# Kernel tuning notes

Measured on AMD Instinct MI355X. Metric: run time of the kernel, lower is better.

Reference implementation:

```python
import jax, jax.numpy as jnp
import numpy as np

N = 32000      # total nodes (16 graphs x 2000 nodes)
B = 16         # batch of graphs
NPG = N // B   # nodes per graph
K = 1600       # assign_dim (total clusters)
KPG = K // B   # clusters per graph
D = 128        # input_dim == output_feat_dim
E = 512000     # edges (avg degree 16), block-diagonal across graphs


def setup_inputs() -> dict:
    key = jax.random.key(0)
    ks = jax.random.split(key, 12)
    # block-structured edge list: each edge stays within its graph
    epg = E // B
    gid = jnp.repeat(jnp.arange(B, dtype=jnp.int32), epg) * NPG
    src = gid + jax.random.randint(ks[0], (E,), 0, NPG, dtype=jnp.int32)
    dst = gid + jax.random.randint(ks[1], (E,), 0, NPG, dtype=jnp.int32)
    h = jax.random.normal(ks[2], (N, D), dtype=jnp.float32)
    s = 0.05
    return {
        'h': h, 'src': src, 'dst': dst,
        'W1f': jax.random.normal(ks[3], (D, D), jnp.float32) * s,
        'b1f': jnp.zeros((D,), jnp.float32),
        'W2f': jax.random.normal(ks[4], (D, D), jnp.float32) * s,
        'b2f': jnp.zeros((D,), jnp.float32),
        'W1p': jax.random.normal(ks[5], (D, K), jnp.float32) * s,
        'b1p': jnp.zeros((K,), jnp.float32),
        'W2p': jax.random.normal(ks[6], (K, K), jnp.float32) * s,
        'b2p': jnp.zeros((K,), jnp.float32),
    }


def _gin(h, src, dst, W1, b1, W2, b2):
    # mean-aggregate neighbor features, then 2-layer MLP (histocartography GINLayer)
    deg = jax.ops.segment_sum(jnp.ones((src.shape[0],), h.dtype), dst, num_segments=N)
    agg = jax.ops.segment_sum(h[src], dst, num_segments=N)
    agg = agg / jnp.maximum(deg, 1.0)[:, None]
    x = h + agg
    x = jax.nn.relu(x @ W1 + b1)
    x = jax.nn.relu(x @ W2 + b2)
    return x


def _forward(h, src, dst, W1f, b1f, W2f, b2f, W1p, b1p, W2p, b2p):
    feat = _gin(h, src, dst, W1f, b1f, W2f, b2f)            # [N, D]
    assign = _gin(h, src, dst, W1p, b1p, W2p, b2p)          # [N, K]
    # block-diagonal mask: node of graph b can only assign to clusters of graph b
    node_gid = jnp.arange(N, dtype=jnp.int32) // NPG
    col_gid = jnp.arange(K, dtype=jnp.int32) // KPG
    mask = (node_gid[:, None] == col_gid[None, :]).astype(assign.dtype)  # [N, K]
    # masked_softmax(memory_efficient=False): softmax(x*mask)*mask, renormalized
    p = jax.nn.softmax(assign * mask, axis=-1) * mask
    assign = p / (jnp.sum(p, axis=-1, keepdims=True) + 1e-13)
    h_pool = assign.T @ feat                                # [K, D]
    # adj @ assign where adj[dst, src] = 1 (sparse-dense mm via scatter)
    tmp = jax.ops.segment_sum(assign[src], dst, num_segments=N)  # [N, K]
    adj_new = assign.T @ tmp                                # [K, K]
    return adj_new, h_pool


def reference(h, src, dst, W1f, b1f, W2f, b2f, W1p, b1p, W2p, b2p):
    return _forward(h, src, dst, W1f, b1f, W2f, b2f, W1p, b1p, W2p, b2p)
```

## Files before the change

kernel.cpp:

```cpp
#include <hip/hip_runtime.h>

#define N_NODES 32000
#define NPG     2000
#define NGRAPH  16
#define K_ASSIGN 1600
#define KPG     100
#define D_FEAT  128
#define N_EDGES 512000

typedef float f32x4 __attribute__((ext_vector_type(4)));
typedef __bf16 bf16x8 __attribute__((ext_vector_type(8)));

union FragU { unsigned u[4]; bf16x8 v; };

__device__ __forceinline__ float frelu(float v) { return fmaxf(v, 0.0f); }

__device__ __forceinline__ unsigned short f2bf(float f) {
  unsigned u = __float_as_uint(f);
  u += 0x7FFFu + ((u >> 16) & 1u);
  return (unsigned short)(u >> 16);
}
__device__ __forceinline__ float bfLO(unsigned v) { return __uint_as_float(v << 16); }
__device__ __forceinline__ float bfHI(unsigned v) { return __uint_as_float(v & 0xFFFF0000u); }

__global__ __launch_bounds__(256) void prep_all(
    const float* __restrict__ W1f, const float* __restrict__ W2f,
    const float* __restrict__ W1p, const float* __restrict__ W2p,
    unsigned short* __restrict__ o1, unsigned short* __restrict__ o2,
    unsigned short* __restrict__ o3, unsigned short* __restrict__ o4,
    const float* __restrict__ h, unsigned short* __restrict__ h_bf,
    const int* __restrict__ dst, int* __restrict__ cnt) {
  __shared__ float tile[32][33];
  int b = blockIdx.x;
  int t = threadIdx.x;
  if (b >= 6732) {
    int e = (b - 6732) * 256 + t;
    if (e < N_EDGES) atomicAdd(&cnt[dst[e]], 1);
    return;
  }
  if (b >= 2732) {
    int i = (b - 2732) * 256 + t;
    float4 v = ((const float4*)h)[i];
    ushort4 o;
    o.x = f2bf(v.x); o.y = f2bf(v.y); o.z = f2bf(v.z); o.w = f2bf(v.w);
    ((ushort4*)h_bf)[i] = o;
    return;
  }
  const float* in;
  unsigned short* out;
  int R, C, rb;
  if (b < 16)       { in = W1f; out = o1; R = 128;  C = 128;  rb = b; }
  else if (b < 32)  { in = W2f; out = o2; R = 128;  C = 128;  rb = b - 16; }
  else if (b < 232) { in = W1p; out = o3; R = 128;  C = 1600; rb = b - 32; }
  else              { in = W2p; out = o4; R = 1600; C = 1600; rb = b - 232; }
  int ct = C >> 5;
  int bc = rb % ct, br = rb / ct;
  int r0 = br * 32, c0 = bc * 32;
#pragma unroll
  for (int i = 0; i < 4; i++) {
    int r = (t >> 5) + i * 8, c = t & 31;
    tile[r][c] = in[(size_t)(r0 + r) * C + c0 + c];
  }
  __syncthreads();
#pragma unroll
  for (int i = 0; i < 4; i++) {
    int c = (t >> 5) + i * 8, r = t & 31;
    out[(size_t)(c0 + c) * R + r0 + r] = f2bf(tile[r][c]);
  }
}

__global__ __launch_bounds__(1024) void scan_counts(
    const int* __restrict__ cnt, int* __restrict__ rowstart) {
  __shared__ int sums[1024];
  int t = threadIdx.x;
  int base = t * 32;
  int s = 0;
  if (t < 1000)
    for (int i = 0; i < 32; i++) s += cnt[base + i];
  sums[t] = s;
  __syncthreads();
  for (int off = 1; off < 1024; off <<= 1) {
    int v = (t >= off) ? sums[t - off] : 0;
    __syncthreads();
    sums[t] += v;
    __syncthreads();
  }
  if (t < 1000) {
    int run = (t == 0) ? 0 : sums[t - 1];
    for (int i = 0; i < 32; i++) {
      rowstart[base + i] = run;
      run += cnt[base + i];
    }
  }
  if (t == 999) rowstart[32000] = sums[999];
}

__global__ __launch_bounds__(256) void edge_fill(
    const int* __restrict__ src, const int* __restrict__ dst,
    const int* __restrict__ rowstart, int* __restrict__ cursor,
    int* __restrict__ bucket) {
  int e = blockIdx.x * 256 + threadIdx.x;
  if (e < N_EDGES) {
    int d = dst[e];
    int pos = atomicAdd(&cursor[d], 1);
    bucket[rowstart[d] + pos] = src[e];
  }
}

__global__ __launch_bounds__(256) void gin_gather(
    const int* __restrict__ rowstart, const int* __restrict__ bucket,
    const unsigned short* __restrict__ h_bf, unsigned short* __restrict__ x_bf) {
  int bid = (int)(blockIdx.x & 7) * 1000 + (int)(blockIdx.x >> 3);
  int n = bid * 4 + (threadIdx.x >> 6);
  int lane = threadIdx.x & 63;
  int rs = rowstart[n], re = rowstart[n + 1];
  int deg = re - rs;
  const unsigned* hb = (const unsigned*)h_bf;
  unsigned hv = hb[(size_t)n * 64 + lane];
  float ax = 0.f, ay = 0.f;
  for (int base = 0; base < deg; base += 64) {
    int cnt = deg - base;
    if (cnt > 64) cnt = 64;
    int myidx = (lane < cnt) ? bucket[rs + base + lane] : 0;
    int j = 0;
    for (; j + 8 <= cnt; j += 8) {
      int s0 = __shfl(myidx, j + 0), s1 = __shfl(myidx, j + 1);
      int s2 = __shfl(myidx, j + 2), s3 = __shfl(myidx, j + 3);
      int s4 = __shfl(myidx, j + 4), s5 = __shfl(myidx, j + 5);
      int s6 = __shfl(myidx, j + 6), s7 = __shfl(myidx, j + 7);
      unsigned v0 = hb[(size_t)s0 * 64 + lane];
      unsigned v1 = hb[(size_t)s1 * 64 + lane];
      unsigned v2 = hb[(size_t)s2 * 64 + lane];
      unsigned v3 = hb[(size_t)s3 * 64 + lane];
      unsigned v4 = hb[(size_t)s4 * 64 + lane];
      unsigned v5 = hb[(size_t)s5 * 64 + lane];
      unsigned v6 = hb[(size_t)s6 * 64 + lane];
      unsigned v7 = hb[(size_t)s7 * 64 + lane];
      ax += ((bfLO(v0) + bfLO(v1)) + (bfLO(v2) + bfLO(v3))) +
            ((bfLO(v4) + bfLO(v5)) + (bfLO(v6) + bfLO(v7)));
      ay += ((bfHI(v0) + bfHI(v1)) + (bfHI(v2) + bfHI(v3))) +
            ((bfHI(v4) + bfHI(v5)) + (bfHI(v6) + bfHI(v7)));
    }
    for (; j < cnt; j++) {
      int s0 = __shfl(myidx, j);
      unsigned v = hb[(size_t)s0 * 64 + lane];
      ax += bfLO(v);
      ay += bfHI(v);
    }
  }
  float invd = 1.0f / fmaxf((float)deg, 1.0f);
  unsigned o = ((unsigned)f2bf(bfHI(hv) + ay * invd) << 16) |
               f2bf(bfLO(hv) + ax * invd);
  ((unsigned*)x_bf)[(size_t)n * 64 + lane] = o;
}

#define FF_STR 136
#define FA_WS 136
#define FA_PS 72
#define FA_W1OFF 17408
#define FA_W2BASE 34816
#define FA_W2OFF 16128
__global__ __launch_bounds__(512) void feat_assign(
    const unsigned short* __restrict__ x_bf,
    const unsigned short* __restrict__ w1ft, const float* __restrict__ b1f,
    const unsigned short* __restrict__ w2ft, const float* __restrict__ b2f,
    unsigned short* __restrict__ feat_bf,
    const unsigned short* __restrict__ w1t, const float* __restrict__ b1p,
    const unsigned short* __restrict__ w2t, const float* __restrict__ b2p,
    unsigned short* __restrict__ assign_bf) {
  __shared__ __align__(16) unsigned char smem[69632];
  int t = threadIdx.x;
  int w = t >> 6, l = t & 63, lr = l & 15, lg = l >> 4;

  if (blockIdx.x >= 256) {
    unsigned short* xa = (unsigned short*)smem;
    unsigned short* ws = (unsigned short*)(smem + 34816);
    size_t base = (size_t)(blockIdx.x - 256) * 128;

#pragma unroll
    for (int i = 0; i < 4; i++) {
      int fi = t + 512 * i;
      int r = fi >> 4, u8 = (fi & 15) * 8;
      *(uint4*)&xa[r * FF_STR + u8] = *(const uint4*)(x_bf + (base + r) * 128 + u8);
      *(uint4*)&ws[r * FF_STR + u8] = *(const uint4*)(w1ft + (size_t)r * 128 + u8);
    }
    __syncthreads();

    int myrow = 16 * w + lr;
    bf16x8 af[4];
#pragma unroll
    for (int kc = 0; kc < 4; kc++)
      af[kc] = *(bf16x8*)&xa[myrow * FF_STR + 32 * kc + 8 * lg];

    f32x4 p[8];
#pragma unroll
    for (int ntk = 0; ntk < 8; ntk++) {
      p[ntk] = (f32x4){0.f, 0.f, 0.f, 0.f};
      int c = 16 * ntk + lr;
#pragma unroll
      for (int kc = 0; kc < 4; kc++) {
        bf16x8 wf = *(bf16x8*)&ws[c * FF_STR + 32 * kc + 8 * lg];
        p[ntk] = __builtin_amdgcn_mfma_f32_16x16x32_bf16(wf, af[kc], p[ntk], 0, 0, 0);
      }
    }
    __syncthreads();

#pragma unroll
    for (int ntk = 0; ntk < 8; ntk++) {
      int kk0 = 16 * ntk + 4 * lg;
      float4 b1 = *(const float4*)(b1f + kk0);
      ushort4 pk;
      pk.x = f2bf(frelu(p[ntk][0] + b1.x));
      pk.y = f2bf(frelu(p[ntk][1] + b1.y));
      pk.z = f2bf(frelu(p[ntk][2] + b1.z));
      pk.w = f2bf(frelu(p[ntk][3] + b1.w));
      *(ushort4*)&xa[myrow * FF_STR + kk0] = pk;
    }
#pragma unroll
    for (int i = 0; i < 4; i++) {
      int fi = t + 512 * i;
      int r = fi >> 4, u8 = (fi & 15) * 8;
      *(uint4*)&ws[r * FF_STR + u8] = *(const uint4*)(w2ft + (size_t)r * 128 + u8);
    }
    __syncthreads();

    bf16x8 a2[4];
#pragma unroll
    for (int kc = 0; kc < 4; kc++)
      a2[kc] = *(bf16x8*)&xa[myrow * FF_STR + 32 * kc + 8 * lg];
#pragma unroll
    for (int nt = 0; nt < 8; nt++) {
      f32x4 q = (f32x4){0.f, 0.f, 0.f, 0.f};
      int c = 16 * nt + lr;
#pragma unroll
      for (int kc = 0; kc < 4; kc++) {
        bf16x8 wf = *(bf16x8*)&ws[c * FF_STR + 32 * kc + 8 * lg];
        q = __builtin_amdgcn_mfma_f32_16x16x32_bf16(wf, a2[kc], q, 0, 0, 0);
      }
      int c0 = 16 * nt + 4 * lg;
      float4 b2 = *(const float4*)(b2f + c0);
      ushort4 pk;
      pk.x = f2bf(frelu(q[0] + b2.x));
      pk.y = f2bf(frelu(q[1] + b2.y));
      pk.z = f2bf(frelu(q[2] + b2.z));
      pk.w = f2bf(frelu(q[3] + b2.w));
      *(ushort4*)&feat_bf[(base + myrow) * 128 + c0] = pk;
    }
    return;
  }

  unsigned short* xt = (unsigned short*)smem;
  int g = blockIdx.x >> 4;
  int row0 = (blockIdx.x & 15) << 7;
  int n0 = g * NPG + row0;

#pragma unroll
  for (int i = 0; i < 4; i++) {
    int fi = t + 512 * i;
    int r = fi >> 4, u8 = (fi & 15) * 8;
    uint4 v = make_uint4(0, 0, 0, 0);
    if (row0 + r < NPG) v = *(const uint4*)(x_bf + (size_t)(n0 + r) * 128 + u8);
    *(uint4*)&xt[r * FA_WS + u8] = v;
  }
  __syncthreads();

  int rh = w >> 1, h = w & 1;

  bf16x8 af[2][4];
#pragma unroll
  for (int ct = 0; ct < 2; ct++)
#pragma unroll
    for (int kc = 0; kc < 4; kc++)
      af[ct][kc] =
          *(bf16x8*)&xt[(32 * rh + 16 * ct + lr) * FA_WS + 32 * kc + 8 * lg];
  __syncthreads();

  {
    unsigned short* w1s = (unsigned short*)smem;
    unsigned short* w2s = (unsigned short*)(smem + FA_W2BASE);
#pragma unroll
    for (int i = 0; i < 2; i++) {
      int fi = t + 512 * i;
      int c = fi >> 4, u8 = (fi & 15) * 8;
      *(uint4*)&w1s[c * FA_WS + u8] = *(const uint4*)(w1t + (size_t)c * 128 + u8);
    }
#pragma unroll
    for (int i = 0; i < 2; i++) {
      int fi = t + 512 * i;
      if (fi < 896) {
        int c = fi >> 3, u8 = (fi & 7) * 8;
        uint4 v = make_uint4(0, 0, 0, 0);
        if (c < KPG)
          v = *(const uint4*)(w2t + (size_t)(g * KPG + c) * K_ASSIGN + u8);
        *(uint4*)&w2s[c * FA_PS + u8] = v;
      }
    }
  }
  __syncthreads();

  f32x4 acc[7][2];
#pragma unroll
  for (int i = 0; i < 7; i++) {
    acc[i][0] = (f32x4){0.f, 0.f, 0.f, 0.f};
    acc[i][1] = (f32x4){0.f, 0.f, 0.f, 0.f};
  }

  for (int cch = 0; cch < 25; cch++) {
    int cur = cch & 1;
    int k0 = cch * 64;
    const unsigned short* w1c = (const unsigned short*)(smem + cur * FA_W1OFF);
    const unsigned short* w2c =
        (const unsigned short*)(smem + FA_W2BASE + cur * FA_W2OFF);
    bool pf = (cch < 24);
    uint4 rA[2], rB[2];
    if (pf) {
      int k1 = k0 + 64;
#pragma unroll
      for (int i = 0; i < 2; i++) {
        int fi = t + 512 * i;
        int c = fi >> 4, u8 = (fi & 15) * 8;
        rA[i] = *(const uint4*)(w1t + (size_t)(k1 + c) * 128 + u8);
      }
#pragma unroll
      for (int i = 0; i < 2; i++) {
        int fi = t + 512 * i;
        rB[i] = make_uint4(0, 0, 0, 0);
        if (fi < 896) {
          int c = fi >> 3, u8 = (fi & 7) * 8;
          if (c < KPG)
            rB[i] = *(const uint4*)(w2t + (size_t)(g * KPG + c) * K_ASSIGN +
                                    k1 + u8);
        }
      }
    }

    f32x4 p[2][2];
    __builtin_amdgcn_s_setprio(1);
#pragma unroll
    for (int nt2 = 0; nt2 < 2; nt2++) {
      p[nt2][0] = (f32x4){0.f, 0.f, 0.f, 0.f};
      p[nt2][1] = (f32x4){0.f, 0.f, 0.f, 0.f};
      int nt = 2 * h + nt2;
#pragma unroll
      for (int kc = 0; kc < 4; kc++) {
        bf16x8 wf = *(bf16x8*)&w1c[(16 * nt + lr) * FA_WS + 32 * kc + 8 * lg];
        p[nt2][0] = __builtin_amdgcn_mfma_f32_16x16x32_bf16(wf, af[0][kc],
                                                            p[nt2][0], 0, 0, 0);
        p[nt2][1] = __builtin_amdgcn_mfma_f32_16x16x32_bf16(wf, af[1][kc],
                                                            p[nt2][1], 0, 0, 0);
      }
    }
    __builtin_amdgcn_s_setprio(0);
    unsigned q[2][2][2];
#pragma unroll
    for (int nt2 = 0; nt2 < 2; nt2++) {
      int kkb = k0 + 16 * (2 * h + nt2) + 4 * lg;
      float4 b1 = *(const float4*)(b1p + kkb);
#pragma unroll
      for (int ct = 0; ct < 2; ct++) {
        float r0 = frelu(p[nt2][ct][0] + b1.x);
        float r1 = frelu(p[nt2][ct][1] + b1.y);
        float r2 = frelu(p[nt2][ct][2] + b1.z);
        float r3 = frelu(p[nt2][ct][3] + b1.w);
        q[nt2][ct][0] = ((unsigned)f2bf(r1) << 16) | f2bf(r0);
        q[nt2][ct][1] = ((unsigned)f2bf(r3) << 16) | f2bf(r2);
      }
    }
    int sA = lr + 32 * (lg & 1);
    int sB = sA + 16;
    bool hi = (lg >= 2);
    FragU pa[2];
#pragma unroll
    for (int ct = 0; ct < 2; ct++) {
      unsigned a0 = (unsigned)__shfl((int)q[0][ct][0], sA, 64);
      unsigned b0 = (unsigned)__shfl((int)q[1][ct][0], sA, 64);
      unsigned a1 = (unsigned)__shfl((int)q[0][ct][1], sA, 64);
      unsigned b1u = (unsigned)__shfl((int)q[1][ct][1], sA, 64);
      unsigned a2 = (unsigned)__shfl((int)q[0][ct][0], sB, 64);
      unsigned b2u = (unsigned)__shfl((int)q[1][ct][0], sB, 64);
      unsigned a3 = (unsigned)__shfl((int)q[0][ct][1], sB, 64);
      unsigned b3u = (unsigned)__shfl((int)q[1][ct][1], sB, 64);
      pa[ct].u[0] = hi ? b0 : a0;
      pa[ct].u[1] = hi ? b1u : a1;
      pa[ct].u[2] = hi ? b2u : a2;
      pa[ct].u[3] = hi ? b3u : a3;
    }
    if (pf) {
      unsigned short* w1n = (unsigned short*)(smem + (cur ^ 1) * FA_W1OFF);
      unsigned short* w2n =
          (unsigned short*)(smem + FA_W2BASE + (cur ^ 1) * FA_W2OFF);
#pragma unroll
      for (int i = 0; i < 2; i++) {
        int fi = t + 512 * i;
        int c = fi >> 4, u8 = (fi & 15) * 8;
        *(uint4*)&w1n[c * FA_WS + u8] = rA[i];
      }
#pragma unroll
      for (int i = 0; i < 2; i++) {
        int fi = t + 512 * i;
        if (fi < 896) {
          int c = fi >> 3, u8 = (fi & 7) * 8;
          *(uint4*)&w2n[c * FA_PS + u8] = rB[i];
        }
      }
    }
    __builtin_amdgcn_s_setprio(1);
#pragma unroll
    for (int ct2 = 0; ct2 < 7; ct2++) {
      bf16x8 wv = *(bf16x8*)&w2c[(16 * ct2 + lr) * FA_PS + 32 * h + 8 * lg];
      acc[ct2][0] = __builtin_amdgcn_mfma_f32_16x16x32_bf16(wv, pa[0].v,
                                                            acc[ct2][0], 0, 0, 0);
      acc[ct2][1] = __builtin_amdgcn_mfma_f32_16x16x32_bf16(wv, pa[1].v,
                                                            acc[ct2][1], 0, 0, 0);
    }
    __builtin_amdgcn_s_setprio(0);
    __syncthreads();
  }

  float* red = (float*)smem;
  if (h == 1) {
#pragma unroll
    for (int ct2 = 0; ct2 < 7; ct2++)
#pragma unroll
      for (int ct = 0; ct < 2; ct++)
        *(f32x4*)&red[((rh * 14 + ct2 * 2 + ct) * 64 + l) * 4] = acc[ct2][ct];
  }
  __syncthreads();
  if (h == 0) {
#pragma unroll
    for (int ct2 = 0; ct2 < 7; ct2++)
#pragma unroll
      for (int ct = 0; ct < 2; ct++)
        acc[ct2][ct] += *(f32x4*)&red[((rh * 14 + ct2 * 2 + ct) * 64 + l) * 4];

#pragma unroll
    for (int ct = 0; ct < 2; ct++) {
      int xrow = row0 + 32 * rh + 16 * ct + lr;
      float v[7][4];
      float m = 0.0f;
#pragma unroll
      for (int ct2 = 0; ct2 < 7; ct2++) {
        int col0 = 16 * ct2 + 4 * lg;
        if (col0 < KPG) {
          float4 b2 = *(const float4*)(b2p + g * KPG + col0);
          v[ct2][0] = frelu(acc[ct2][ct][0] + b2.x);
          v[ct2][1] = frelu(acc[ct2][ct][1] + b2.y);
          v[ct2][2] = frelu(acc[ct2][ct][2] + b2.z);
          v[ct2][3] = frelu(acc[ct2][ct][3] + b2.w);
          m = fmaxf(m, fmaxf(fmaxf(v[ct2][0], v[ct2][1]),
                             fmaxf(v[ct2][2], v[ct2][3])));
        }
      }
      m = fmaxf(m, __shfl_xor(m, 16, 64));
      m = fmaxf(m, __shfl_xor(m, 32, 64));
      float s = 0.0f;
#pragma unroll
      for (int ct2 = 0; ct2 < 7; ct2++) {
        int col0 = 16 * ct2 + 4 * lg;
        if (col0 < KPG) {
          v[ct2][0] = expf(v[ct2][0] - m);
          v[ct2][1] = expf(v[ct2][1] - m);
          v[ct2][2] = expf(v[ct2][2] - m);
          v[ct2][3] = expf(v[ct2][3] - m);
          s += (v[ct2][0] + v[ct2][1]) + (v[ct2][2] + v[ct2][3]);
        }
      }
      s += __shfl_xor(s, 16, 64);
      s += __shfl_xor(s, 32, 64);
      float denom = s + (float)(K_ASSIGN - KPG) * expf(-m);
      float scale = 1.0f / (s + 1e-13f * denom);
      if (xrow < NPG) {
#pragma unroll
        for (int ct2 = 0; ct2 < 7; ct2++) {
          int col0 = 16 * ct2 + 4 * lg;
          if (col0 < KPG) {
            ushort4 pk;
            pk.x = f2bf(v[ct2][0] * scale);
            pk.y = f2bf(v[ct2][1] * scale);
            pk.z = f2bf(v[ct2][2] * scale);
            pk.w = f2bf(v[ct2][3] * scale);
            *(ushort4*)(assign_bf + ((size_t)g * NPG + xrow) * KPG + col0) = pk;
          }
        }
      }
    }
  }
}

__global__ __launch_bounds__(256) void tmp_gather(
    const int* __restrict__ rowstart, const int* __restrict__ bucket,
    const unsigned short* __restrict__ assign_bf, unsigned short* __restrict__ tmp_bf) {
  int bid = (int)(blockIdx.x & 7) * 1000 + (int)(blockIdx.x >> 3);
  int n = bid * 4 + (threadIdx.x >> 6);
  int lane = threadIdx.x & 63;
  int rs = rowstart[n], re = rowstart[n + 1];
  int deg = re - rs;
  int lc = (lane < 50) ? lane : 0;
  const unsigned* ab = (const unsigned*)assign_bf;
  float ax = 0.f, ay = 0.f;
  for (int base = 0; base < deg; base += 64) {
    int cnt = deg - base;
    if (cnt > 64) cnt = 64;
    int myidx = (lane < cnt) ? bucket[rs + base + lane] : 0;
    int j = 0;
    for (; j + 8 <= cnt; j += 8) {
      int s0 = __shfl(myidx, j + 0), s1 = __shfl(myidx, j + 1);
      int s2 = __shfl(myidx, j + 2), s3 = __shfl(myidx, j + 3);
      int s4 = __shfl(myidx, j + 4), s5 = __shfl(myidx, j + 5);
      int s6 = __shfl(myidx, j + 6), s7 = __shfl(myidx, j + 7);
      unsigned v0 = ab[(size_t)s0 * 50 + lc];
      unsigned v1 = ab[(size_t)s1 * 50 + lc];
      unsigned v2 = ab[(size_t)s2 * 50 + lc];
      unsigned v3 = ab[(size_t)s3 * 50 + lc];
      unsigned v4 = ab[(size_t)s4 * 50 + lc];
      unsigned v5 = ab[(size_t)s5 * 50 + lc];
      unsigned v6 = ab[(size_t)s6 * 50 + lc];
      unsigned v7 = ab[(size_t)s7 * 50 + lc];
      ax += ((bfLO(v0) + bfLO(v1)) + (bfLO(v2) + bfLO(v3))) +
            ((bfLO(v4) + bfLO(v5)) + (bfLO(v6) + bfLO(v7)));
      ay += ((bfHI(v0) + bfHI(v1)) + (bfHI(v2) + bfHI(v3))) +
            ((bfHI(v4) + bfHI(v5)) + (bfHI(v6) + bfHI(v7)));
    }
    for (; j < cnt; j++) {
      int s0 = __shfl(myidx, j);
      unsigned v = ab[(size_t)s0 * 50 + lc];
      ax += bfLO(v);
      ay += bfHI(v);
    }
  }
  if (lane < 50) {
    unsigned o = ((unsigned)f2bf(ay) << 16) | f2bf(ax);
    ((unsigned*)tmp_bf)[(size_t)n * 50 + lane] = o;
  }
}

#define PA_STR 72
#define PA_CHN 128
__global__ __launch_bounds__(256) void pool_adj_mfma(
    const unsigned short* __restrict__ assign_bf,
    const unsigned short* __restrict__ feat_bf,
    const unsigned short* __restrict__ tmp_bf,
    float* __restrict__ out_adj, float* __restrict__ out_hpool) {
  __shared__ __align__(16) unsigned short as[112 * PA_STR];
  __shared__ __align__(16) unsigned short bs[128 * PA_STR];
  bool is_pool = blockIdx.x < 256;
  int bb = is_pool ? blockIdx.x : blockIdx.x - 256;
  int g = bb >> 4, ch = bb & 15;
  int nbase = ch * PA_CHN;
  int lim = NPG - nbase;
  if (lim > PA_CHN) lim = PA_CHN;
  int t = threadIdx.x;
  int w = t >> 6, l = t & 63, lr = l & 15, lg = l >> 4;
  const unsigned* au = (const unsigned*)assign_bf;
  const unsigned* fu = (const unsigned*)feat_bf;
  const unsigned* tu = (const unsigned*)tmp_bf;

  for (int i = t; i < 12 * PA_STR; i += 256) as[100 * PA_STR + i] = 0;
  for (int i = t; i < 28 * PA_STR; i += 256) bs[100 * PA_STR + i] = 0;

  f32x4 acc[7][2];
#pragma unroll
  for (int i = 0; i < 7; i++) {
    acc[i][0] = (f32x4){0.f, 0.f, 0.f, 0.f};
    acc[i][1] = (f32x4){0.f, 0.f, 0.f, 0.f};
  }

  for (int kt = 0; kt < 2; kt++) {
    int nt0 = kt * 64;
    __syncthreads();
#pragma unroll
    for (int i = 0; i < 13; i++) {
      int idx = t + 256 * i;
      if (idx < 3200) {
        int r = idx / 50, cu = idx % 50;
        int nl = nt0 + r;
        unsigned v = 0;
        if (nl < lim) v = au[(size_t)(g * NPG + nbase + nl) * 50 + cu];
        as[(2 * cu) * PA_STR + r] = (unsigned short)(v & 0xFFFFu);
        as[(2 * cu + 1) * PA_STR + r] = (unsigned short)(v >> 16);
      }
    }
    if (is_pool) {
#pragma unroll
      for (int i = 0; i < 16; i++) {
        int idx = t + 256 * i;
        int r = idx >> 6, cu = idx & 63;
        int nl = nt0 + r;
        unsigned v = 0;
        if (nl < lim) v = fu[(size_t)(g * NPG + nbase + nl) * 64 + cu];
        bs[(2 * cu) * PA_STR + r] = (unsigned short)(v & 0xFFFFu);
        bs[(2 * cu + 1) * PA_STR + r] = (unsigned short)(v >> 16);
      }
    } else {
#pragma unroll
      for (int i = 0; i < 13; i++) {
        int idx = t + 256 * i;
        if (idx < 3200) {
          int r = idx / 50, cu = idx % 50;
          int nl = nt0 + r;
          unsigned v = 0;
          if (nl < lim) v = tu[(size_t)(g * NPG + nbase + nl) * 50 + cu];
          bs[(2 * cu) * PA_STR + r] = (unsigned short)(v & 0xFFFFu);
          bs[(2 * cu + 1) * PA_STR + r] = (unsigned short)(v >> 16);
        }
      }
    }
    __syncthreads();
#pragma unroll
    for (int kc = 0; kc < 2; kc++) {
      bf16x8 afr[7];
#pragma unroll
      for (int mt = 0; mt < 7; mt++)
        afr[mt] = *(bf16x8*)&as[(16 * mt + lr) * PA_STR + 32 * kc + 8 * lg];
#pragma unroll
      for (int nt2 = 0; nt2 < 2; nt2++) {
        int nt = 2 * w + nt2;
        bf16x8 bfr = *(bf16x8*)&bs[(16 * nt + lr) * PA_STR + 32 * kc + 8 * lg];
#pragma unroll
        for (int mt = 0; mt < 7; mt++)
          acc[mt][nt2] =
              __builtin_amdgcn_mfma_f32_16x16x32_bf16(afr[mt], bfr, acc[mt][nt2], 0, 0, 0);
      }
    }
  }

  if (is_pool) {
#pragma unroll
    for (int mt = 0; mt < 7; mt++)
#pragma unroll
      for (int nt2 = 0; nt2 < 2; nt2++) {
        int nt = 2 * w + nt2;
#pragma unroll
        for (int r = 0; r < 4; r++) {
          int m = 16 * mt + 4 * lg + r;
          if (m < KPG)
            atomicAdd(out_hpool + ((size_t)g * KPG + m) * 128 + 16 * nt + lr,
                      acc[mt][nt2][r]);
        }
      }
  } else {
#pragma unroll
    for (int mt = 0; mt < 7; mt++)
#pragma unroll
      for (int nt2 = 0; nt2 < 2; nt2++) {
        int nt = 2 * w + nt2;
        if (nt < 7) {
          int k2 = 16 * nt + lr;
          if (k2 < KPG) {
#pragma unroll
            for (int r = 0; r < 4; r++) {
              int m = 16 * mt + 4 * lg + r;
              if (m < KPG)
                atomicAdd(out_adj + ((size_t)g * KPG + m) * K_ASSIGN + g * KPG + k2,
                          acc[mt][nt2][r]);
            }
          }
        }
      }
  }
}

extern "C" void kernel_launch(void* const* d_in, const int* in_sizes, int n_in,
                              void* d_out, int out_size, void* d_ws,
                              size_t ws_size, hipStream_t stream) {
  (void)in_sizes; (void)n_in; (void)ws_size;
  const float* h   = (const float*)d_in[0];
  const int*   src = (const int*)d_in[1];
  const int*   dst = (const int*)d_in[2];
  const float* W1f = (const float*)d_in[3];
  const float* b1f = (const float*)d_in[4];
  const float* W2f = (const float*)d_in[5];
  const float* b2f = (const float*)d_in[6];
  const float* W1p = (const float*)d_in[7];
  const float* b1p = (const float*)d_in[8];
  const float* W2p = (const float*)d_in[9];
  const float* b2p = (const float*)d_in[10];

  float* out_adj   = (float*)d_out;
  float* out_hpool = out_adj + (size_t)K_ASSIGN * K_ASSIGN;

  char* ws = (char*)d_ws;
  int* deg_cnt  = (int*)(ws + 0);
  int* rowstart = (int*)(ws + 128000);
  int* cursor   = (int*)(ws + 256032);
  int* bucket   = (int*)(ws + 384032);
  unsigned short* h_bf      = (unsigned short*)(ws + 2432032);
  unsigned short* x_bf      = (unsigned short*)(ws + 10624032);
  unsigned short* feat_bf   = (unsigned short*)(ws + 18816032);
  unsigned short* assign_bf = (unsigned short*)(ws + 27008032);
  unsigned short* tmp_bf    = (unsigned short*)(ws + 33408032);
  unsigned short* w1f_t     = (unsigned short*)(ws + 39808032);
  unsigned short* w2f_t     = (unsigned short*)(ws + 39840800);
  unsigned short* w1p_t     = (unsigned short*)(ws + 39873568);
  unsigned short* w2p_t     = (unsigned short*)(ws + 40283168);

  hipMemsetAsync(deg_cnt, 0, 128000, stream);
  hipMemsetAsync(cursor, 0, 128000, stream);
  hipMemsetAsync(d_out, 0, (size_t)out_size * sizeof(float), stream);

  prep_all<<<8732, 256, 0, stream>>>(W1f, W2f, W1p, W2p, w1f_t, w2f_t, w1p_t,
                                     w2p_t, h, h_bf, dst, deg_cnt);

  scan_counts<<<1, 1024, 0, stream>>>(deg_cnt, rowstart);
  edge_fill<<<N_EDGES / 256, 256, 0, stream>>>(src, dst, rowstart, cursor, bucket);

  gin_gather<<<N_NODES / 4, 256, 0, stream>>>(rowstart, bucket, h_bf, x_bf);

  feat_assign<<<256 + N_NODES / 128, 512, 0, stream>>>(
      x_bf, w1f_t, b1f, w2f_t, b2f, feat_bf,
      w1p_t, b1p, w2p_t, b2p, assign_bf);

  tmp_gather<<<N_NODES / 4, 256, 0, stream>>>(rowstart, bucket, assign_bf, tmp_bf);

  pool_adj_mfma<<<512, 256, 0, stream>>>(assign_bf, feat_bf, tmp_bf,
                                         out_adj, out_hpool);
}
```

Baseline: 216.5 us.

## Fuse neighbor-mean gather into feat_assign, dropping the separate x_bf pass

Removes the standalone gin_gather kernel and its x_bf buffer. Each feat_assign block now computes its own rows of x (h plus the mean of its neighbors) directly into shared memory before the MLP matmuls, with each wave gathering 16 rows. This saves one kernel launch and a global write and re-read of x. In exchange the feat and assign blocks each redo the same gather (256 + 250 blocks over the same nodes), and the gather now runs inside a kernel that has 512 threads per block and a large shared-memory footprint, which may reduce latency hiding.

```diff
diff --git a/kernel.cpp b/kernel.cpp
--- a/kernel.cpp
+++ b/kernel.cpp
@@ -23,99 +23,11 @@
 __device__ __forceinline__ float bfLO(unsigned v) { return __uint_as_float(v << 16); }
 __device__ __forceinline__ float bfHI(unsigned v) { return __uint_as_float(v & 0xFFFF0000u); }
 
-__global__ __launch_bounds__(256) void prep_all(
-    const float* __restrict__ W1f, const float* __restrict__ W2f,
-    const float* __restrict__ W1p, const float* __restrict__ W2p,
-    unsigned short* __restrict__ o1, unsigned short* __restrict__ o2,
-    unsigned short* __restrict__ o3, unsigned short* __restrict__ o4,
-    const float* __restrict__ h, unsigned short* __restrict__ h_bf,
-    const int* __restrict__ dst, int* __restrict__ cnt) {
-  __shared__ float tile[32][33];
-  int b = blockIdx.x;
-  int t = threadIdx.x;
-  if (b >= 6732) {
-    int e = (b - 6732) * 256 + t;
-    if (e < N_EDGES) atomicAdd(&cnt[dst[e]], 1);
-    return;
-  }
-  if (b >= 2732) {
-    int i = (b - 2732) * 256 + t;
-    float4 v = ((const float4*)h)[i];
-    ushort4 o;
-    o.x = f2bf(v.x); o.y = f2bf(v.y); o.z = f2bf(v.z); o.w = f2bf(v.w);
-    ((ushort4*)h_bf)[i] = o;
-    return;
-  }
-  const float* in;
-  unsigned short* out;
-  int R, C, rb;
-  if (b < 16)       { in = W1f; out = o1; R = 128;  C = 128;  rb = b; }
-  else if (b < 32)  { in = W2f; out = o2; R = 128;  C = 128;  rb = b - 16; }
-  else if (b < 232) { in = W1p; out = o3; R = 128;  C = 1600; rb = b - 32; }
-  else              { in = W2p; out = o4; R = 1600; C = 1600; rb = b - 232; }
-  int ct = C >> 5;
-  int bc = rb % ct, br = rb / ct;
-  int r0 = br * 32, c0 = bc * 32;
-#pragma unroll
-  for (int i = 0; i < 4; i++) {
-    int r = (t >> 5) + i * 8, c = t & 31;
-    tile[r][c] = in[(size_t)(r0 + r) * C + c0 + c];
-  }
-  __syncthreads();
-#pragma unroll
-  for (int i = 0; i < 4; i++) {
-    int c = (t >> 5) + i * 8, r = t & 31;
-    out[(size_t)(c0 + c) * R + r0 + r] = f2bf(tile[r][c]);
-  }
-}
-
-__global__ __launch_bounds__(1024) void scan_counts(
-    const int* __restrict__ cnt, int* __restrict__ rowstart) {
-  __shared__ int sums[1024];
-  int t = threadIdx.x;
-  int base = t * 32;
-  int s = 0;
-  if (t < 1000)
-    for (int i = 0; i < 32; i++) s += cnt[base + i];
-  sums[t] = s;
-  __syncthreads();
-  for (int off = 1; off < 1024; off <<= 1) {
-    int v = (t >= off) ? sums[t - off] : 0;
-    __syncthreads();
-    sums[t] += v;
-    __syncthreads();
-  }
-  if (t < 1000) {
-    int run = (t == 0) ? 0 : sums[t - 1];
-    for (int i = 0; i < 32; i++) {
-      rowstart[base + i] = run;
-      run += cnt[base + i];
-    }
-  }
-  if (t == 999) rowstart[32000] = sums[999];
-}
-
-__global__ __launch_bounds__(256) void edge_fill(
-    const int* __restrict__ src, const int* __restrict__ dst,
-    const int* __restrict__ rowstart, int* __restrict__ cursor,
-    int* __restrict__ bucket) {
-  int e = blockIdx.x * 256 + threadIdx.x;
-  if (e < N_EDGES) {
-    int d = dst[e];
-    int pos = atomicAdd(&cursor[d], 1);
-    bucket[rowstart[d] + pos] = src[e];
-  }
-}
-
-__global__ __launch_bounds__(256) void gin_gather(
-    const int* __restrict__ rowstart, const int* __restrict__ bucket,
-    const unsigned short* __restrict__ h_bf, unsigned short* __restrict__ x_bf) {
-  int bid = (int)(blockIdx.x & 7) * 1000 + (int)(blockIdx.x >> 3);
-  int n = bid * 4 + (threadIdx.x >> 6);
-  int lane = threadIdx.x & 63;
+__device__ __forceinline__ unsigned gather_x_u32(
+    int n, int lane, const int* __restrict__ rowstart,
+    const int* __restrict__ bucket, const unsigned* __restrict__ hb) {
   int rs = rowstart[n], re = rowstart[n + 1];
   int deg = re - rs;
-  const unsigned* hb = (const unsigned*)h_bf;
   unsigned hv = hb[(size_t)n * 64 + lane];
   float ax = 0.f, ay = 0.f;
   for (int base = 0; base < deg; base += 64) {
@@ -149,9 +61,92 @@
     }
   }
   float invd = 1.0f / fmaxf((float)deg, 1.0f);
-  unsigned o = ((unsigned)f2bf(bfHI(hv) + ay * invd) << 16) |
-               f2bf(bfLO(hv) + ax * invd);
-  ((unsigned*)x_bf)[(size_t)n * 64 + lane] = o;
+  return ((unsigned)f2bf(bfHI(hv) + ay * invd) << 16) |
+         f2bf(bfLO(hv) + ax * invd);
+}
+
+__global__ __launch_bounds__(256) void prep_all(
+    const float* __restrict__ W1f, const float* __restrict__ W2f,
+    const float* __restrict__ W1p, const float* __restrict__ W2p,
+    unsigned short* __restrict__ o1, unsigned short* __restrict__ o2,
+    unsigned short* __restrict__ o3, unsigned short* __restrict__ o4,
+    const float* __restrict__ h, unsigned short* __restrict__ h_bf,
+    const int* __restrict__ dst, int* __restrict__ cnt) {
+  __shared__ float tile[32][33];
+  int b = blockIdx.x;
+  int t = threadIdx.x;
+  if (b >= 6732) {
+    int e = (b - 6732) * 256 + t;
+    if (e < N_EDGES) atomicAdd(&cnt[dst[e]], 1);
+    return;
+  }
+  if (b >= 2732) {
+    int i = (b - 2732) * 256 + t;
+    float4 v = ((const float4*)h)[i];
+    ushort4 o;
+    o.x = f2bf(v.x); o.y = f2bf(v.y); o.z = f2bf(v.z); o.w = f2bf(v.w);
+    ((ushort4*)h_bf)[i] = o;
+    return;
+  }
+  const float* in;
+  unsigned short* out;
+  int R, C, rb;
+  if (b < 16)       { in = W1f; out = o1; R = 128;  C = 128;  rb = b; }
+  else if (b < 32)  { in = W2f; out = o2; R = 128;  C = 128;  rb = b - 16; }
+  else if (b < 232) { in = W1p; out = o3; R = 128;  C = 1600; rb = b - 32; }
+  else              { in = W2p; out = o4; R = 1600; C = 1600; rb = b - 232; }
+  int ct = C >> 5;
+  int bc = rb % ct, br = rb / ct;
+  int r0 = br * 32, c0 = bc * 32;
+#pragma unroll
+  for (int i = 0; i < 4; i++) {
+    int r = (t >> 5) + i * 8, c = t & 31;
+    tile[r][c] = in[(size_t)(r0 + r) * C + c0 + c];
+  }
+  __syncthreads();
+#pragma unroll
+  for (int i = 0; i < 4; i++) {
+    int c = (t >> 5) + i * 8, r = t & 31;
+    out[(size_t)(c0 + c) * R + r0 + r] = f2bf(tile[r][c]);
+  }
+}
+
+__global__ __launch_bounds__(1024) void scan_counts(
+    const int* __restrict__ cnt, int* __restrict__ rowstart) {
+  __shared__ int sums[1024];
+  int t = threadIdx.x;
+  int base = t * 32;
+  int s = 0;
+  if (t < 1000)
+    for (int i = 0; i < 32; i++) s += cnt[base + i];
+  sums[t] = s;
+  __syncthreads();
+  for (int off = 1; off < 1024; off <<= 1) {
+    int v = (t >= off) ? sums[t - off] : 0;
+    __syncthreads();
+    sums[t] += v;
+    __syncthreads();
+  }
+  if (t < 1000) {
+    int run = (t == 0) ? 0 : sums[t - 1];
+    for (int i = 0; i < 32; i++) {
+      rowstart[base + i] = run;
+      run += cnt[base + i];
+    }
+  }
+  if (t == 999) rowstart[32000] = sums[999];
+}
+
+__global__ __launch_bounds__(256) void edge_fill(
+    const int* __restrict__ src, const int* __restrict__ dst,
+    const int* __restrict__ rowstart, int* __restrict__ cursor,
+    int* __restrict__ bucket) {
+  int e = blockIdx.x * 256 + threadIdx.x;
+  if (e < N_EDGES) {
+    int d = dst[e];
+    int pos = atomicAdd(&cursor[d], 1);
+    bucket[rowstart[d] + pos] = src[e];
+  }
 }
 
 #define FF_STR 136
@@ -161,7 +156,8 @@
 #define FA_W2BASE 34816
 #define FA_W2OFF 16128
 __global__ __launch_bounds__(512) void feat_assign(
-    const unsigned short* __restrict__ x_bf,
+    const int* __restrict__ rowstart, const int* __restrict__ bucket,
+    const unsigned short* __restrict__ h_bf,
     const unsigned short* __restrict__ w1ft, const float* __restrict__ b1f,
     const unsigned short* __restrict__ w2ft, const float* __restrict__ b2f,
     unsigned short* __restrict__ feat_bf,
@@ -171,6 +167,7 @@
   __shared__ __align__(16) unsigned char smem[69632];
   int t = threadIdx.x;
   int w = t >> 6, l = t & 63, lr = l & 15, lg = l >> 4;
+  const unsigned* hb = (const unsigned*)h_bf;
 
   if (blockIdx.x >= 256) {
     unsigned short* xa = (unsigned short*)smem;
@@ -181,8 +178,12 @@
     for (int i = 0; i < 4; i++) {
       int fi = t + 512 * i;
       int r = fi >> 4, u8 = (fi & 15) * 8;
-      *(uint4*)&xa[r * FF_STR + u8] = *(const uint4*)(x_bf + (base + r) * 128 + u8);
       *(uint4*)&ws[r * FF_STR + u8] = *(const uint4*)(w1ft + (size_t)r * 128 + u8);
+    }
+    for (int j = 0; j < 16; j++) {
+      int r = 16 * w + j;
+      unsigned o = gather_x_u32((int)base + r, l, rowstart, bucket, hb);
+      *(unsigned*)&xa[r * FF_STR + l * 2] = o;
     }
     __syncthreads();
 
@@ -254,13 +255,11 @@
   int row0 = (blockIdx.x & 15) << 7;
   int n0 = g * NPG + row0;
 
-#pragma unroll
-  for (int i = 0; i < 4; i++) {
-    int fi = t + 512 * i;
-    int r = fi >> 4, u8 = (fi & 15) * 8;
-    uint4 v = make_uint4(0, 0, 0, 0);
-    if (row0 + r < NPG) v = *(const uint4*)(x_bf + (size_t)(n0 + r) * 128 + u8);
-    *(uint4*)&xt[r * FA_WS + u8] = v;
+  for (int j = 0; j < 16; j++) {
+    int r = 16 * w + j;
+    unsigned o = 0;
+    if (row0 + r < NPG) o = gather_x_u32(n0 + r, l, rowstart, bucket, hb);
+    *(unsigned*)&xt[r * FA_WS + l * 2] = o;
   }
   __syncthreads();
 
@@ -685,14 +684,13 @@
   int* cursor   = (int*)(ws + 256032);
   int* bucket   = (int*)(ws + 384032);
   unsigned short* h_bf      = (unsigned short*)(ws + 2432032);
-  unsigned short* x_bf      = (unsigned short*)(ws + 10624032);
-  unsigned short* feat_bf   = (unsigned short*)(ws + 18816032);
-  unsigned short* assign_bf = (unsigned short*)(ws + 27008032);
-  unsigned short* tmp_bf    = (unsigned short*)(ws + 33408032);
-  unsigned short* w1f_t     = (unsigned short*)(ws + 39808032);
-  unsigned short* w2f_t     = (unsigned short*)(ws + 39840800);
-  unsigned short* w1p_t     = (unsigned short*)(ws + 39873568);
-  unsigned short* w2p_t     = (unsigned short*)(ws + 40283168);
+  unsigned short* feat_bf   = (unsigned short*)(ws + 10624032);
+  unsigned short* assign_bf = (unsigned short*)(ws + 18816032);
+  unsigned short* tmp_bf    = (unsigned short*)(ws + 25216032);
+  unsigned short* w1f_t     = (unsigned short*)(ws + 31616032);
+  unsigned short* w2f_t     = (unsigned short*)(ws + 31648800);
+  unsigned short* w1p_t     = (unsigned short*)(ws + 31681568);
+  unsigned short* w2p_t     = (unsigned short*)(ws + 32091168);
 
   hipMemsetAsync(deg_cnt, 0, 128000, stream);
   hipMemsetAsync(cursor, 0, 128000, stream);
@@ -704,10 +702,9 @@
   scan_counts<<<1, 1024, 0, stream>>>(deg_cnt, rowstart);
   edge_fill<<<N_EDGES / 256, 256, 0, stream>>>(src, dst, rowstart, cursor, bucket);
 
-  gin_gather<<<N_NODES / 4, 256, 0, stream>>>(rowstart, bucket, h_bf, x_bf);
-
   feat_assign<<<256 + N_NODES / 128, 512, 0, stream>>>(
-      x_bf, w1f_t, b1f, w2f_t, b2f, feat_bf,
+      rowstart, bucket, h_bf,
+      w1f_t, b1f, w2f_t, b2f, feat_bf,
       w1p_t, b1p, w2p_t, b2p, assign_bf);
 
   tmp_gather<<<N_NODES / 4, 256, 0, stream>>>(rowstart, bucket, assign_bf, tmp_bf);
```

Measured after the change: 286.2 us. +32.2%, slower.

## Load GIN weight fragments directly from global memory instead of LDS staging

Applied to the files above, without the earlier changes.

Removes LDS staging and double buffering of the W1/W2 weights in both the feature and assignment MLP paths. Each wave now loads its MFMA weight fragments straight from global memory, relying on L2/cache reuse. This drops most per-chunk __syncthreads and halves shared memory use, which may raise occupancy. The trade-off is redundant global loads per wave and no explicit prefetch, and the reduction is split into two smaller passes.

```diff
diff --git a/kernel.cpp b/kernel.cpp
--- a/kernel.cpp
+++ b/kernel.cpp
@@ -156,10 +156,6 @@
 
 #define FF_STR 136
 #define FA_WS 136
-#define FA_PS 72
-#define FA_W1OFF 17408
-#define FA_W2BASE 34816
-#define FA_W2OFF 16128
 __global__ __launch_bounds__(512) void feat_assign(
     const unsigned short* __restrict__ x_bf,
     const unsigned short* __restrict__ w1ft, const float* __restrict__ b1f,
@@ -168,24 +164,19 @@
     const unsigned short* __restrict__ w1t, const float* __restrict__ b1p,
     const unsigned short* __restrict__ w2t, const float* __restrict__ b2p,
     unsigned short* __restrict__ assign_bf) {
-  __shared__ __align__(16) unsigned char smem[69632];
+  __shared__ __align__(16) unsigned char smem[34816];
   int t = threadIdx.x;
   int w = t >> 6, l = t & 63, lr = l & 15, lg = l >> 4;
 
   if (blockIdx.x >= 256) {
     unsigned short* xa = (unsigned short*)smem;
-    unsigned short* ws = (unsigned short*)(smem + 34816);
     size_t base = (size_t)(blockIdx.x - 256) * 128;
-
-#pragma unroll
-    for (int i = 0; i < 4; i++) {
-      int fi = t + 512 * i;
-      int r = fi >> 4, u8 = (fi & 15) * 8;
+#pragma unroll
+    for (int j = 0; j < 4; j++) {
+      int idx = l + 64 * j;
+      int r = 16 * w + (idx >> 4), u8 = (idx & 15) * 8;
       *(uint4*)&xa[r * FF_STR + u8] = *(const uint4*)(x_bf + (base + r) * 128 + u8);
-      *(uint4*)&ws[r * FF_STR + u8] = *(const uint4*)(w1ft + (size_t)r * 128 + u8);
-    }
-    __syncthreads();
-
+    }
     int myrow = 16 * w + lr;
     bf16x8 af[4];
 #pragma unroll
@@ -195,16 +186,16 @@
     f32x4 p[8];
 #pragma unroll
     for (int ntk = 0; ntk < 8; ntk++) {
+      int c = 16 * ntk + lr;
+      bf16x8 wfr[4];
+#pragma unroll
+      for (int kc = 0; kc < 4; kc++)
+        wfr[kc] = *(const bf16x8*)(w1ft + (size_t)c * 128 + 32 * kc + 8 * lg);
       p[ntk] = (f32x4){0.f, 0.f, 0.f, 0.f};
-      int c = 16 * ntk + lr;
-#pragma unroll
-      for (int kc = 0; kc < 4; kc++) {
-        bf16x8 wf = *(bf16x8*)&ws[c * FF_STR + 32 * kc + 8 * lg];
-        p[ntk] = __builtin_amdgcn_mfma_f32_16x16x32_bf16(wf, af[kc], p[ntk], 0, 0, 0);
-      }
-    }
-    __syncthreads();
-
+#pragma unroll
+      for (int kc = 0; kc < 4; kc++)
+        p[ntk] = __builtin_amdgcn_mfma_f32_16x16x32_bf16(wfr[kc], af[kc], p[ntk], 0, 0, 0);
+    }
 #pragma unroll
     for (int ntk = 0; ntk < 8; ntk++) {
       int kk0 = 16 * ntk + 4 * lg;
@@ -216,27 +207,21 @@
       pk.w = f2bf(frelu(p[ntk][3] + b1.w));
       *(ushort4*)&xa[myrow * FF_STR + kk0] = pk;
     }
-#pragma unroll
-    for (int i = 0; i < 4; i++) {
-      int fi = t + 512 * i;
-      int r = fi >> 4, u8 = (fi & 15) * 8;
-      *(uint4*)&ws[r * FF_STR + u8] = *(const uint4*)(w2ft + (size_t)r * 128 + u8);
-    }
-    __syncthreads();
-
     bf16x8 a2[4];
 #pragma unroll
     for (int kc = 0; kc < 4; kc++)
       a2[kc] = *(bf16x8*)&xa[myrow * FF_STR + 32 * kc + 8 * lg];
 #pragma unroll
     for (int nt = 0; nt < 8; nt++) {
+      int c = 16 * nt + lr;
+      bf16x8 wfr[4];
+#pragma unroll
+      for (int kc = 0; kc < 4; kc++)
+        wfr[kc] = *(const bf16x8*)(w2ft + (size_t)c * 128 + 32 * kc + 8 * lg);
       f32x4 q = (f32x4){0.f, 0.f, 0.f, 0.f};
-      int c = 16 * nt + lr;
-#pragma unroll
-      for (int kc = 0; kc < 4; kc++) {
-        bf16x8 wf = *(bf16x8*)&ws[c * FF_STR + 32 * kc + 8 * lg];
-        q = __builtin_amdgcn_mfma_f32_16x16x32_bf16(wf, a2[kc], q, 0, 0, 0);
-      }
+#pragma unroll
+      for (int kc = 0; kc < 4; kc++)
+        q = __builtin_amdgcn_mfma_f32_16x16x32_bf16(wfr[kc], a2[kc], q, 0, 0, 0);
       int c0 = 16 * nt + 4 * lg;
       float4 b2 = *(const float4*)(b2f + c0);
       ushort4 pk;
@@ -264,7 +249,7 @@
   }
   __syncthreads();
 
-  int rh = w >> 1, h = w & 1;
+  int rh = w >> 1, hh = w & 1;
 
   bf16x8 af[2][4];
 #pragma unroll
@@ -273,30 +258,6 @@
     for (int kc = 0; kc < 4; kc++)
       af[ct][kc] =
           *(bf16x8*)&xt[(32 * rh + 16 * ct + lr) * FA_WS + 32 * kc + 8 * lg];
-  __syncthreads();
-
-  {
-    unsigned short* w1s = (unsigned short*)smem;
-    unsigned short* w2s = (unsigned short*)(smem + FA_W2BASE);
-#pragma unroll
-    for (int i = 0; i < 2; i++) {
-      int fi = t + 512 * i;
-      int c = fi >> 4, u8 = (fi & 15) * 8;
-      *(uint4*)&w1s[c * FA_WS + u8] = *(const uint4*)(w1t + (size_t)c * 128 + u8);
-    }
-#pragma unroll
-    for (int i = 0; i < 2; i++) {
-      int fi = t + 512 * i;
-      if (fi < 896) {
-        int c = fi >> 3, u8 = (fi & 7) * 8;
-        uint4 v = make_uint4(0, 0, 0, 0);
-        if (c < KPG)
-          v = *(const uint4*)(w2t + (size_t)(g * KPG + c) * K_ASSIGN + u8);
-        *(uint4*)&w2s[c * FA_PS + u8] = v;
-      }
-    }
-  }
-  __syncthreads();
 
   f32x4 acc[7][2];
 #pragma unroll
@@ -306,47 +267,23 @@
   }
 
   for (int cch = 0; cch < 25; cch++) {
-    int cur = cch & 1;
     int k0 = cch * 64;
-    const unsigned short* w1c = (const unsigned short*)(smem + cur * FA_W1OFF);
-    const unsigned short* w2c =
-        (const unsigned short*)(smem + FA_W2BASE + cur * FA_W2OFF);
-    bool pf = (cch < 24);
-    uint4 rA[2], rB[2];
-    if (pf) {
-      int k1 = k0 + 64;
-#pragma unroll
-      for (int i = 0; i < 2; i++) {
-        int fi = t + 512 * i;
-        int c = fi >> 4, u8 = (fi & 15) * 8;
-        rA[i] = *(const uint4*)(w1t + (size_t)(k1 + c) * 128 + u8);
-      }
-#pragma unroll
-      for (int i = 0; i < 2; i++) {
-        int fi = t + 512 * i;
-        rB[i] = make_uint4(0, 0, 0, 0);
-        if (fi < 896) {
-          int c = fi >> 3, u8 = (fi & 7) * 8;
-          if (c < KPG)
-            rB[i] = *(const uint4*)(w2t + (size_t)(g * KPG + c) * K_ASSIGN +
-                                    k1 + u8);
-        }
-      }
-    }
-
     f32x4 p[2][2];
     __builtin_amdgcn_s_setprio(1);
 #pragma unroll
     for (int nt2 = 0; nt2 < 2; nt2++) {
+      bf16x8 wfr[4];
+#pragma unroll
+      for (int kc = 0; kc < 4; kc++)
+        wfr[kc] = *(const bf16x8*)(
+            w1t + (size_t)(k0 + 16 * (2 * hh + nt2) + lr) * 128 + 32 * kc + 8 * lg);
       p[nt2][0] = (f32x4){0.f, 0.f, 0.f, 0.f};
       p[nt2][1] = (f32x4){0.f, 0.f, 0.f, 0.f};
-      int nt = 2 * h + nt2;
 #pragma unroll
       for (int kc = 0; kc < 4; kc++) {
-        bf16x8 wf = *(bf16x8*)&w1c[(16 * nt + lr) * FA_WS + 32 * kc + 8 * lg];
-        p[nt2][0] = __builtin_amdgcn_mfma_f32_16x16x32_bf16(wf, af[0][kc],
+        p[nt2][0] = __builtin_amdgcn_mfma_f32_16x16x32_bf16(wfr[kc], af[0][kc],
                                                             p[nt2][0], 0, 0, 0);
-        p[nt2][1] = __builtin_amdgcn_mfma_f32_16x16x32_bf16(wf, af[1][kc],
+        p[nt2][1] = __builtin_amdgcn_mfma_f32_16x16x32_bf16(wfr[kc], af[1][kc],
                                                             p[nt2][1], 0, 0, 0);
       }
     }
@@ -354,7 +291,7 @@
     unsigned q[2][2][2];
 #pragma unroll
     for (int nt2 = 0; nt2 < 2; nt2++) {
-      int kkb = k0 + 16 * (2 * h + nt2) + 4 * lg;
+      int kkb = k0 + 16 * (2 * hh + nt2) + 4 * lg;
       float4 b1 = *(const float4*)(b1p + kkb);
 #pragma unroll
       for (int ct = 0; ct < 2; ct++) {
@@ -385,56 +322,36 @@
       pa[ct].u[2] = hi ? b2u : a2;
       pa[ct].u[3] = hi ? b3u : a3;
     }
-    if (pf) {
-      unsigned short* w1n = (unsigned short*)(smem + (cur ^ 1) * FA_W1OFF);
-      unsigned short* w2n =
-          (unsigned short*)(smem + FA_W2BASE + (cur ^ 1) * FA_W2OFF);
-#pragma unroll
-      for (int i = 0; i < 2; i++) {
-        int fi = t + 512 * i;
-        int c = fi >> 4, u8 = (fi & 15) * 8;
-        *(uint4*)&w1n[c * FA_WS + u8] = rA[i];
-      }
-#pragma unroll
-      for (int i = 0; i < 2; i++) {
-        int fi = t + 512 * i;
-        if (fi < 896) {
-          int c = fi >> 3, u8 = (fi & 7) * 8;
-          *(uint4*)&w2n[c * FA_PS + u8] = rB[i];
-        }
-      }
-    }
     __builtin_amdgcn_s_setprio(1);
 #pragma unroll
     for (int ct2 = 0; ct2 < 7; ct2++) {
-      bf16x8 wv = *(bf16x8*)&w2c[(16 * ct2 + lr) * FA_PS + 32 * h + 8 * lg];
+      int c = 16 * ct2 + lr;
+      int crow = g * KPG + (c < KPG ? c : KPG - 1);
+      bf16x8 wv = *(const bf16x8*)(
+          w2t + (size_t)crow * K_ASSIGN + k0 + 32 * hh + 8 * lg);
       acc[ct2][0] = __builtin_amdgcn_mfma_f32_16x16x32_bf16(wv, pa[0].v,
                                                             acc[ct2][0], 0, 0, 0);
       acc[ct2][1] = __builtin_amdgcn_mfma_f32_16x16x32_bf16(wv, pa[1].v,
                                                             acc[ct2][1], 0, 0, 0);
     }
     __builtin_amdgcn_s_setprio(0);
+  }
+
+  float* red = (float*)smem;
+#pragma unroll
+  for (int ct = 0; ct < 2; ct++) {
     __syncthreads();
-  }
-
-  float* red = (float*)smem;
-  if (h == 1) {
-#pragma unroll
-    for (int ct2 = 0; ct2 < 7; ct2++)
-#pragma unroll
-      for (int ct = 0; ct < 2; ct++)
-        *(f32x4*)&red[((rh * 14 + ct2 * 2 + ct) * 64 + l) * 4] = acc[ct2][ct];
-  }
-  __syncthreads();
-  if (h == 0) {
-#pragma unroll
-    for (int ct2 = 0; ct2 < 7; ct2++)
-#pragma unroll
-      for (int ct = 0; ct < 2; ct++)
-        acc[ct2][ct] += *(f32x4*)&red[((rh * 14 + ct2 * 2 + ct) * 64 + l) * 4];
-
-#pragma unroll
-    for (int ct = 0; ct < 2; ct++) {
+    if (hh == 1) {
+#pragma unroll
+      for (int ct2 = 0; ct2 < 7; ct2++)
+        *(f32x4*)&red[((rh * 7 + ct2) * 64 + l) * 4] = acc[ct2][ct];
+    }
+    __syncthreads();
+    if (hh == 0) {
+#pragma unroll
+      for (int ct2 = 0; ct2 < 7; ct2++)
+        acc[ct2][ct] += *(f32x4*)&red[((rh * 7 + ct2) * 64 + l) * 4];
+
       int xrow = row0 + 32 * rh + 16 * ct + lr;
       float v[7][4];
       float m = 0.0f;
```

After: 288.7 us. 33.3% more time.
